# Kernel optimization log

Measured on AMD Instinct MI355X. Metric: run time of the kernel, lower is better.

## Reference

```python
import jax, jax.numpy as jnp
import numpy as np

N, P, Q, T, J, B, H = 262144, 64, 64, 2048, 512, 8, 64


def setup_inputs() -> dict:
    key = jax.random.key(0)
    ks = jax.random.split(key, 11)
    sH = 1.0 / np.sqrt(H).astype(np.float32)
    return {
        "idx": jax.random.randint(ks[0], (B,), 0, J),
        "seg_ids": jnp.sort(jax.random.randint(ks[1], (N,), 0, T)),
        "K": jax.random.normal(ks[2], (N, P), jnp.float32) * 0.1,
        "V": jax.random.normal(ks[3], (N, Q), jnp.float32),
        "S": jax.random.normal(ks[4], (P, J), jnp.float32) * 0.1,
        "W_ih": jax.random.normal(ks[5], (3 * H, Q), jnp.float32) * sH,
        "W_hh": jax.random.normal(ks[6], (3 * H, H), jnp.float32) * sH,
        "b_ih": jax.random.normal(ks[7], (3 * H,), jnp.float32) * sH,
        "b_hh": jax.random.normal(ks[8], (3 * H,), jnp.float32) * sH,
        "w_out": jax.random.normal(ks[9], (1, H), jnp.float32) * sH,
        "b_out": jax.random.normal(ks[10], (1,), jnp.float32) * sH,
    }


def reference(idx, seg_ids, K, V, S, W_ih, W_hh, b_ih, b_hh, w_out, b_out):
    # W[:, b] = K @ S[:, idx[b]]  -> [N, B]
    w = K @ S[:, idx]
    # ragged per-segment softmax over the N axis (segments = date windows)
    m = jax.ops.segment_max(w, seg_ids, num_segments=T)          # [T, B]
    e = jnp.exp(w - m[seg_ids])                                  # [N, B]
    denom = jax.ops.segment_sum(e, seg_ids, num_segments=T)     # [T, B]
    alpha = e / denom[seg_ids]                                   # [N, B]
    # weighted aggregation of V rows per segment: M[t, b] = sum_u alpha_u * V_u
    M = jax.ops.segment_sum(alpha[:, :, None] * V[:, None, :],
                            seg_ids, num_segments=T)             # [T, B, Q]
    X = jnp.transpose(M, (1, 0, 2))                              # [B, T, Q]

    # PyTorch GRU (gate order r,z,n). Faithful to the original bug: GRU was
    # built without batch_first=True, so axis 0 (B) is time, axis 1 (T) is batch.
    def step(h, x_t):  # x_t: [T, Q], h: [T, H]
        gi = x_t @ W_ih.T + b_ih                                 # [T, 3H]
        gh = h @ W_hh.T + b_hh                                   # [T, 3H]
        i_r, i_z, i_n = jnp.split(gi, 3, axis=1)
        h_r, h_z, h_n = jnp.split(gh, 3, axis=1)
        r = jax.nn.sigmoid(i_r + h_r)
        z = jax.nn.sigmoid(i_z + h_z)
        n = jnp.tanh(i_n + r * h_n)
        h_new = (1.0 - z) * n + z * h
        return h_new, h_new

    h0 = jnp.zeros((T, H), X.dtype)
    _, hs = jax.lax.scan(step, h0, X)                            # [B, T, H]
    preds = hs @ w_out.T + b_out                                 # [B, T, 1]
    return preds
```

## Files before the change

### kernel.cpp

```cpp
#include <hip/hip_runtime.h>
#include <math.h>

#define NN 262144
#define PP 64
#define QQ 64
#define TT 2048
#define JJ 512
#define BB 8
#define HH 64

__device__ __forceinline__ float lane_bcast(float v, int l) {
  return __int_as_float(__builtin_amdgcn_readlane(__float_as_int(v), l));
}

__global__ void k_prep(const int* __restrict__ seg_ids, int* __restrict__ seg_start) {
  int tid = blockIdx.x * blockDim.x + threadIdx.x;
  if (tid <= TT) {
    int lo = 0, hi = NN;
    while (lo < hi) {
      int mid = (lo + hi) >> 1;
      if (seg_ids[mid] < tid) lo = mid + 1; else hi = mid;
    }
    seg_start[tid] = lo;
  }
}

#define NPASS 6
__global__ __launch_bounds__(256) void k_fused2(const float* __restrict__ Kmat,
                                                const int* __restrict__ idx,
                                                const float* __restrict__ S,
                                                const float* __restrict__ V,
                                                const int* __restrict__ seg_start,
                                                float* __restrict__ M) {
  __shared__ __align__(16) float s_cols[BB * PP];
  __shared__ __align__(16) float accred[4][8][64];
  __shared__ float reds[4][8];
  int tid = threadIdx.x;
  int t = blockIdx.x;
  for (int i = tid; i < BB * PP; i += 256) {
    int p = i >> 3, b = i & 7;
    s_cols[b * PP + p] = S[p * JJ + idx[b]];
  }
  __syncthreads();

  int s = seg_start[t], e = seg_start[t + 1];
  int lane = tid & 63, j = tid >> 6;
  int len = e - s;
  int chunk = (len + 3) >> 2;
  int b0 = s + j * chunk;
  int b1 = b0 + chunk; if (b1 > e) b1 = e;

  int krow_in = lane >> 2;
  int sub = lane & 3;
  float ewa[NPASS], ewb[NPASS];
#pragma unroll
  for (int p = 0; p < NPASS; ++p) {
    ewa[p] = 0.f; ewb[p] = 0.f;
    int base = b0 + 16 * p;
    if (base < b1) {
      int rp = base + krow_in;
      int rc = (rp < b1) ? rp : (b1 - 1);
      const float4* Kp = reinterpret_cast<const float4*>(Kmat + (size_t)rc * PP + sub * 16);
      float4 kq[4];
#pragma unroll
      for (int jj = 0; jj < 4; ++jj) kq[jj] = Kp[jj];
      float a8[8];
#pragma unroll
      for (int b = 0; b < 8; ++b) a8[b] = 0.f;
#pragma unroll
      for (int j4 = 0; j4 < 4; ++j4) {
        float4 kk = kq[j4];
#pragma unroll
        for (int b = 0; b < 8; ++b) {
          const float4 sv = *reinterpret_cast<const float4*>(&s_cols[b * PP + sub * 16 + j4 * 4]);
          a8[b] += kk.x * sv.x + kk.y * sv.y + kk.z * sv.z + kk.w * sv.w;
        }
      }
#pragma unroll
      for (int b = 0; b < 8; ++b) {
        a8[b] += __shfl_xor(a8[b], 1);
        a8[b] += __shfl_xor(a8[b], 2);
      }
      float ox = (sub == 0) ? a8[0] : (sub == 1) ? a8[2] : (sub == 2) ? a8[4] : a8[6];
      float oy = (sub == 0) ? a8[1] : (sub == 1) ? a8[3] : (sub == 2) ? a8[5] : a8[7];
      ewa[p] = __expf(ox);
      ewb[p] = __expf(oy);
    }
  }

  int rsub = lane >> 4;
  int qg = lane & 15;
  float4 acc[8];
#pragma unroll
  for (int b = 0; b < 8; ++b) acc[b] = make_float4(0.f, 0.f, 0.f, 0.f);
  float4 selo = make_float4(0.f, 0.f, 0.f, 0.f);
  float4 sehi = make_float4(0.f, 0.f, 0.f, 0.f);

#pragma unroll
  for (int p = 0; p < NPASS; ++p) {
    int base = b0 + 16 * p;
    if (base < b1) {
#pragma unroll
      for (int q = 0; q < 4; ++q) {
        int qb = base + 4 * q;
        if (qb < b1) {
          int r = qb + rsub;
          float pr = (r < b1) ? 1.f : 0.f;
          int rc = (r < b1) ? r : (b1 - 1);
          float4 vv = reinterpret_cast<const float4*>(V + (size_t)rc * QQ)[qg];
          int sL = (4 * q + rsub) * 4;
          float e0 = __shfl(ewa[p], sL + 0), e1 = __shfl(ewb[p], sL + 0);
          float e2 = __shfl(ewa[p], sL + 1), e3 = __shfl(ewb[p], sL + 1);
          float e4 = __shfl(ewa[p], sL + 2), e5 = __shfl(ewb[p], sL + 2);
          float e6 = __shfl(ewa[p], sL + 3), e7 = __shfl(ewb[p], sL + 3);
          e0 *= pr; e1 *= pr; e2 *= pr; e3 *= pr;
          e4 *= pr; e5 *= pr; e6 *= pr; e7 *= pr;
          selo.x += e0; selo.y += e1; selo.z += e2; selo.w += e3;
          sehi.x += e4; sehi.y += e5; sehi.z += e6; sehi.w += e7;
          acc[0].x += e0 * vv.x; acc[0].y += e0 * vv.y; acc[0].z += e0 * vv.z; acc[0].w += e0 * vv.w;
          acc[1].x += e1 * vv.x; acc[1].y += e1 * vv.y; acc[1].z += e1 * vv.z; acc[1].w += e1 * vv.w;
          acc[2].x += e2 * vv.x; acc[2].y += e2 * vv.y; acc[2].z += e2 * vv.z; acc[2].w += e2 * vv.w;
          acc[3].x += e3 * vv.x; acc[3].y += e3 * vv.y; acc[3].z += e3 * vv.z; acc[3].w += e3 * vv.w;
          acc[4].x += e4 * vv.x; acc[4].y += e4 * vv.y; acc[4].z += e4 * vv.z; acc[4].w += e4 * vv.w;
          acc[5].x += e5 * vv.x; acc[5].y += e5 * vv.y; acc[5].z += e5 * vv.z; acc[5].w += e5 * vv.w;
          acc[6].x += e6 * vv.x; acc[6].y += e6 * vv.y; acc[6].z += e6 * vv.z; acc[6].w += e6 * vv.w;
          acc[7].x += e7 * vv.x; acc[7].y += e7 * vv.y; acc[7].z += e7 * vv.z; acc[7].w += e7 * vv.w;
        }
      }
    }
  }

#pragma unroll
  for (int b = 0; b < 8; ++b) {
    acc[b].x += __shfl_xor(acc[b].x, 16); acc[b].y += __shfl_xor(acc[b].y, 16);
    acc[b].z += __shfl_xor(acc[b].z, 16); acc[b].w += __shfl_xor(acc[b].w, 16);
    acc[b].x += __shfl_xor(acc[b].x, 32); acc[b].y += __shfl_xor(acc[b].y, 32);
    acc[b].z += __shfl_xor(acc[b].z, 32); acc[b].w += __shfl_xor(acc[b].w, 32);
  }
  selo.x += __shfl_xor(selo.x, 16); selo.y += __shfl_xor(selo.y, 16);
  selo.z += __shfl_xor(selo.z, 16); selo.w += __shfl_xor(selo.w, 16);
  sehi.x += __shfl_xor(sehi.x, 16); sehi.y += __shfl_xor(sehi.y, 16);
  sehi.z += __shfl_xor(sehi.z, 16); sehi.w += __shfl_xor(sehi.w, 16);
  selo.x += __shfl_xor(selo.x, 32); selo.y += __shfl_xor(selo.y, 32);
  selo.z += __shfl_xor(selo.z, 32); selo.w += __shfl_xor(selo.w, 32);
  sehi.x += __shfl_xor(sehi.x, 32); sehi.y += __shfl_xor(sehi.y, 32);
  sehi.z += __shfl_xor(sehi.z, 32); sehi.w += __shfl_xor(sehi.w, 32);

  if (rsub == 0) {
#pragma unroll
    for (int b = 0; b < 8; ++b)
      *reinterpret_cast<float4*>(&accred[j][b][qg * 4]) = acc[b];
    if (qg == 0) {
      reds[j][0] = selo.x; reds[j][1] = selo.y; reds[j][2] = selo.z; reds[j][3] = selo.w;
      reds[j][4] = sehi.x; reds[j][5] = sehi.y; reds[j][6] = sehi.z; reds[j][7] = sehi.w;
    }
  }
  __syncthreads();
  for (int o = tid; o < 512; o += 256) {
    int b = o >> 6, q = o & 63;
    float dd = reds[0][b] + reds[1][b] + reds[2][b] + reds[3][b];
    float inv = (dd > 0.f) ? 1.f / dd : 0.f;
    float sum = accred[0][b][q] + accred[1][b][q] + accred[2][b][q] + accred[3][b][q];
    M[(size_t)t * 512 + o] = sum * inv;
  }
}

__global__ __launch_bounds__(256) void k_gi(const float* __restrict__ M,
                                            const float* __restrict__ W_ih,
                                            const float* __restrict__ b_ih,
                                            float* __restrict__ GI) {
  __shared__ float Wt[64 * 193];
  int tid = threadIdx.x;
  for (int i = tid; i < 192 * 64; i += 256) {
    int g = i >> 6, k = i & 63;
    Wt[k * 193 + g] = W_ih[i];
  }
  __syncthreads();
  int lane = tid & 63, wv = tid >> 6;
  int row0 = blockIdx.x * 32 + wv * 8;
  float x[8];
#pragma unroll
  for (int rr = 0; rr < 8; ++rr) {
    int rho = row0 + rr;
    int b = rho >> 11, t = rho & 2047;
    x[rr] = M[((size_t)t * 8 + b) * 64 + lane];
  }
  float bi0 = b_ih[lane], bi1 = b_ih[64 + lane], bi2 = b_ih[128 + lane];
  float a0[8], a1[8], a2[8];
#pragma unroll
  for (int rr = 0; rr < 8; ++rr) { a0[rr] = bi0; a1[rr] = bi1; a2[rr] = bi2; }
#pragma unroll
  for (int k = 0; k < 64; ++k) {
    float w0 = Wt[k * 193 + lane];
    float w1 = Wt[k * 193 + 64 + lane];
    float w2 = Wt[k * 193 + 128 + lane];
#pragma unroll
    for (int rr = 0; rr < 8; ++rr) {
      float xk = lane_bcast(x[rr], k);
      a0[rr] += w0 * xk; a1[rr] += w1 * xk; a2[rr] += w2 * xk;
    }
  }
#pragma unroll
  for (int rr = 0; rr < 8; ++rr) {
    size_t rho = (size_t)row0 + rr;
    GI[rho * 192 + lane]       = a0[rr];
    GI[rho * 192 + 64 + lane]  = a1[rr];
    GI[rho * 192 + 128 + lane] = a2[rr];
  }
}

__global__ __launch_bounds__(256) void k_gru(const float* __restrict__ GI,
                                             const float* __restrict__ W_hh,
                                             const float* __restrict__ b_hh,
                                             const float* __restrict__ w_out,
                                             const float* __restrict__ b_out,
                                             float* __restrict__ preds) {
  __shared__ __align__(16) float Wl[192 * 68];
  int tid = threadIdx.x;
  for (int i = tid; i < 192 * 16; i += 256) {
    int g = i >> 4, c = i & 15;
    *reinterpret_cast<float4*>(&Wl[g * 68 + c * 4]) =
        *reinterpret_cast<const float4*>(W_hh + g * 64 + c * 4);
  }
  __syncthreads();
  int lane = tid & 63, wv = tid >> 6;
  int t = blockIdx.x * 4 + wv;
  float bh0 = b_hh[lane], bh1 = b_hh[64 + lane], bh2 = b_hh[128 + lane];
  float wo = w_out[lane];
  float bo = b_out[0];
  const float* w0base = &Wl[lane * 68];
  const float* w1base = &Wl[(64 + lane) * 68];
  const float* w2base = &Wl[(128 + lane) * 68];

  float gr[8], gz[8], gn[8];
#pragma unroll
  for (int b = 0; b < 8; ++b) {
    size_t base = ((size_t)b * TT + t) * 192;
    gr[b] = GI[base + lane];
    gz[b] = GI[base + 64 + lane];
    gn[b] = GI[base + 128 + lane];
  }

  float h;
  {
    float r = 1.f / (1.f + __expf(-(gr[0] + bh0)));
    float z = 1.f / (1.f + __expf(-(gz[0] + bh1)));
    float nv = tanhf(gn[0] + r * bh2);
    h = (1.f - z) * nv;
    float pv = h * wo;
#pragma unroll
    for (int off = 32; off; off >>= 1) pv += __shfl_xor(pv, off);
    if (lane == 0) preds[t] = pv + bo;
  }
#pragma unroll
  for (int b = 1; b < 8; ++b) {
    float ar = bh0, az = bh1, an = bh2;
#pragma unroll
    for (int c = 0; c < 16; ++c) {
      const float4 w0 = *reinterpret_cast<const float4*>(w0base + c * 4);
      const float4 w1 = *reinterpret_cast<const float4*>(w1base + c * 4);
      const float4 w2 = *reinterpret_cast<const float4*>(w2base + c * 4);
      float a0 = lane_bcast(h, c * 4 + 0), a1 = lane_bcast(h, c * 4 + 1);
      float a2 = lane_bcast(h, c * 4 + 2), a3 = lane_bcast(h, c * 4 + 3);
      ar += w0.x * a0 + w0.y * a1 + w0.z * a2 + w0.w * a3;
      az += w1.x * a0 + w1.y * a1 + w1.z * a2 + w1.w * a3;
      an += w2.x * a0 + w2.y * a1 + w2.z * a2 + w2.w * a3;
    }
    float r = 1.f / (1.f + __expf(-(gr[b] + ar)));
    float z = 1.f / (1.f + __expf(-(gz[b] + az)));
    float nv = tanhf(gn[b] + r * an);
    h = (1.f - z) * nv + z * h;
    float pv = h * wo;
#pragma unroll
    for (int off = 32; off; off >>= 1) pv += __shfl_xor(pv, off);
    if (lane == 0) preds[(size_t)b * TT + t] = pv + bo;
  }
}

extern "C" void kernel_launch(void* const* d_in, const int* in_sizes, int n_in,
                              void* d_out, int out_size, void* d_ws, size_t ws_size,
                              hipStream_t stream) {
  const int*   idx     = (const int*)d_in[0];
  const int*   seg_ids = (const int*)d_in[1];
  const float* Kmat    = (const float*)d_in[2];
  const float* V       = (const float*)d_in[3];
  const float* S       = (const float*)d_in[4];
  const float* W_ih    = (const float*)d_in[5];
  const float* W_hh    = (const float*)d_in[6];
  const float* b_ih    = (const float*)d_in[7];
  const float* b_hh    = (const float*)d_in[8];
  const float* w_out   = (const float*)d_in[9];
  const float* b_out   = (const float*)d_in[10];
  float* out = (float*)d_out;

  char* ws = (char*)d_ws;
  int*   seg_start = (int*)(ws + 0);
  float* M  = (float*)(ws + 8448);
  float* GI = (float*)(ws + 4202752);

  hipLaunchKernelGGL(k_prep, dim3(9), dim3(256), 0, stream, seg_ids, seg_start);
  hipLaunchKernelGGL(k_fused2, dim3(TT), dim3(256), 0, stream,
                     Kmat, idx, S, V, seg_start, M);
  hipLaunchKernelGGL(k_gi, dim3(512), dim3(256), 0, stream, M, W_ih, b_ih, GI);
  hipLaunchKernelGGL(k_gru, dim3(512), dim3(256), 0, stream, GI, W_hh, b_hh, w_out, b_out, out);
}
```

Measured before the change: 79.08 us.

## Split segment attention into fixed 64-row blocks with per-block partials and reduction

Replaces the per-segment block (one block per T, variable length) with fixed 64-row blocks over N, each producing up to 3 per-segment partial sums (weighted V and exp sums) into a workspace. A new reduction kernel then combines up to 4 block partials per segment and normalizes. The seg_start binary search is folded into the first kernel. This is meant to remove load imbalance and the NPASS cap, and to make K/V reads fully coalesced. In exchange it adds a ~25MB partial buffer write and read plus an extra launch, and it silently assumes each 64-row block spans at most 3 segments and each segment touches at most 4 blocks.

```diff
diff --git a/kernel.cpp b/kernel.cpp
--- a/kernel.cpp
+++ b/kernel.cpp
@@ -8,160 +8,189 @@
 #define JJ 512
 #define BB 8
 #define HH 64
+#define PSTR 520
 
 __device__ __forceinline__ float lane_bcast(float v, int l) {
   return __int_as_float(__builtin_amdgcn_readlane(__float_as_int(v), l));
 }
 
-__global__ void k_prep(const int* __restrict__ seg_ids, int* __restrict__ seg_start) {
-  int tid = blockIdx.x * blockDim.x + threadIdx.x;
-  if (tid <= TT) {
+__global__ __launch_bounds__(256) void k_fused3(const float* __restrict__ Kmat,
+                                                const int* __restrict__ idx,
+                                                const float* __restrict__ S,
+                                                const float* __restrict__ V,
+                                                const int* __restrict__ seg_ids,
+                                                float* __restrict__ P3,
+                                                int* __restrict__ seg_start) {
+  __shared__ __align__(16) float s_cols[BB * PP];
+  __shared__ __align__(16) float ew_lds[64 * 8];
+  __shared__ int seg_lds[64];
+  __shared__ __align__(16) float accred[4][8][64];
+  __shared__ float reds[4][8];
+  int tid = threadIdx.x;
+  int n0 = blockIdx.x * 64;
+  int gtid = blockIdx.x * 256 + tid;
+  if (gtid <= TT) {
     int lo = 0, hi = NN;
     while (lo < hi) {
       int mid = (lo + hi) >> 1;
-      if (seg_ids[mid] < tid) lo = mid + 1; else hi = mid;
-    }
-    seg_start[tid] = lo;
-  }
-}
-
-#define NPASS 6
-__global__ __launch_bounds__(256) void k_fused2(const float* __restrict__ Kmat,
-                                                const int* __restrict__ idx,
-                                                const float* __restrict__ S,
-                                                const float* __restrict__ V,
-                                                const int* __restrict__ seg_start,
-                                                float* __restrict__ M) {
-  __shared__ __align__(16) float s_cols[BB * PP];
-  __shared__ __align__(16) float accred[4][8][64];
-  __shared__ float reds[4][8];
-  int tid = threadIdx.x;
-  int t = blockIdx.x;
+      if (seg_ids[mid] < gtid) lo = mid + 1; else hi = mid;
+    }
+    seg_start[gtid] = lo;
+  }
+  if (tid < 64) seg_lds[tid] = seg_ids[n0 + tid];
   for (int i = tid; i < BB * PP; i += 256) {
     int p = i >> 3, b = i & 7;
     s_cols[b * PP + p] = S[p * JJ + idx[b]];
   }
-  __syncthreads();
-
+
+  int lane = tid & 63, w = tid >> 6;
+  int rsub = lane >> 4, qg = lane & 15;
+
+  float4 vv[4];
+#pragma unroll
+  for (int qi = 0; qi < 4; ++qi) {
+    int rl = w * 16 + qi * 4 + rsub;
+    vv[qi] = reinterpret_cast<const float4*>(V + (size_t)(n0 + rl) * QQ)[qg];
+  }
+  __syncthreads();
+
+  {
+    int row = tid >> 2;
+    int sub = tid & 3;
+    const float4* Kp = reinterpret_cast<const float4*>(Kmat + (size_t)(n0 + row) * PP + sub * 16);
+    float4 kq[4];
+#pragma unroll
+    for (int j = 0; j < 4; ++j) kq[j] = Kp[j];
+    float a8[8];
+#pragma unroll
+    for (int b = 0; b < 8; ++b) a8[b] = 0.f;
+#pragma unroll
+    for (int j4 = 0; j4 < 4; ++j4) {
+      float4 kk = kq[j4];
+#pragma unroll
+      for (int b = 0; b < 8; ++b) {
+        const float4 sv = *reinterpret_cast<const float4*>(&s_cols[b * PP + sub * 16 + j4 * 4]);
+        a8[b] += kk.x * sv.x + kk.y * sv.y + kk.z * sv.z + kk.w * sv.w;
+      }
+    }
+#pragma unroll
+    for (int b = 0; b < 8; ++b) {
+      a8[b] += __shfl_xor(a8[b], 1);
+      a8[b] += __shfl_xor(a8[b], 2);
+    }
+    float ox = (sub == 0) ? a8[0] : (sub == 1) ? a8[2] : (sub == 2) ? a8[4] : a8[6];
+    float oy = (sub == 0) ? a8[1] : (sub == 1) ? a8[3] : (sub == 2) ? a8[5] : a8[7];
+    *reinterpret_cast<float2*>(&ew_lds[row * 8 + 2 * sub]) =
+        make_float2(__expf(ox), __expf(oy));
+  }
+  __syncthreads();
+
+  int t_lo = seg_lds[0], t_hi = seg_lds[63];
+  int npass = t_hi - t_lo + 1; if (npass > 3) npass = 3;
+  int tq[4];
+#pragma unroll
+  for (int qi = 0; qi < 4; ++qi) tq[qi] = seg_lds[w * 16 + qi * 4 + rsub];
+
+  for (int pi = 0; pi < npass; ++pi) {
+    int tt = t_lo + pi;
+    float4 acc[8];
+#pragma unroll
+    for (int b = 0; b < 8; ++b) acc[b] = make_float4(0.f, 0.f, 0.f, 0.f);
+    float se[8];
+#pragma unroll
+    for (int b = 0; b < 8; ++b) se[b] = 0.f;
+#pragma unroll
+    for (int qi = 0; qi < 4; ++qi) {
+      int rl = w * 16 + qi * 4 + rsub;
+      float wq = (tq[qi] == tt) ? 1.f : 0.f;
+      float4 elo = *reinterpret_cast<const float4*>(&ew_lds[rl * 8]);
+      float4 ehi = *reinterpret_cast<const float4*>(&ew_lds[rl * 8 + 4]);
+      elo.x *= wq; elo.y *= wq; elo.z *= wq; elo.w *= wq;
+      ehi.x *= wq; ehi.y *= wq; ehi.z *= wq; ehi.w *= wq;
+      se[0] += elo.x; se[1] += elo.y; se[2] += elo.z; se[3] += elo.w;
+      se[4] += ehi.x; se[5] += ehi.y; se[6] += ehi.z; se[7] += ehi.w;
+      float4 v4 = vv[qi];
+      acc[0].x += elo.x * v4.x; acc[0].y += elo.x * v4.y; acc[0].z += elo.x * v4.z; acc[0].w += elo.x * v4.w;
+      acc[1].x += elo.y * v4.x; acc[1].y += elo.y * v4.y; acc[1].z += elo.y * v4.z; acc[1].w += elo.y * v4.w;
+      acc[2].x += elo.z * v4.x; acc[2].y += elo.z * v4.y; acc[2].z += elo.z * v4.z; acc[2].w += elo.z * v4.w;
+      acc[3].x += elo.w * v4.x; acc[3].y += elo.w * v4.y; acc[3].z += elo.w * v4.z; acc[3].w += elo.w * v4.w;
+      acc[4].x += ehi.x * v4.x; acc[4].y += ehi.x * v4.y; acc[4].z += ehi.x * v4.z; acc[4].w += ehi.x * v4.w;
+      acc[5].x += ehi.y * v4.x; acc[5].y += ehi.y * v4.y; acc[5].z += ehi.y * v4.z; acc[5].w += ehi.y * v4.w;
+      acc[6].x += ehi.z * v4.x; acc[6].y += ehi.z * v4.y; acc[6].z += ehi.z * v4.z; acc[6].w += ehi.z * v4.w;
+      acc[7].x += ehi.w * v4.x; acc[7].y += ehi.w * v4.y; acc[7].z += ehi.w * v4.z; acc[7].w += ehi.w * v4.w;
+    }
+#pragma unroll
+    for (int b = 0; b < 8; ++b) {
+      acc[b].x += __shfl_xor(acc[b].x, 16); acc[b].y += __shfl_xor(acc[b].y, 16);
+      acc[b].z += __shfl_xor(acc[b].z, 16); acc[b].w += __shfl_xor(acc[b].w, 16);
+      acc[b].x += __shfl_xor(acc[b].x, 32); acc[b].y += __shfl_xor(acc[b].y, 32);
+      acc[b].z += __shfl_xor(acc[b].z, 32); acc[b].w += __shfl_xor(acc[b].w, 32);
+      se[b] += __shfl_xor(se[b], 16);
+      se[b] += __shfl_xor(se[b], 32);
+    }
+    if (rsub == 0) {
+#pragma unroll
+      for (int b = 0; b < 8; ++b)
+        *reinterpret_cast<float4*>(&accred[w][b][qg * 4]) = acc[b];
+      if (qg == 0) {
+#pragma unroll
+        for (int b = 0; b < 8; ++b) reds[w][b] = se[b];
+      }
+    }
+    __syncthreads();
+    float* Pp = P3 + ((size_t)blockIdx.x * 3 + pi) * PSTR;
+    for (int o = tid; o < 512; o += 256) {
+      int b = o >> 6, q = o & 63;
+      Pp[o] = accred[0][b][q] + accred[1][b][q] + accred[2][b][q] + accred[3][b][q];
+    }
+    if (tid < 8)
+      Pp[512 + tid] = reds[0][tid] + reds[1][tid] + reds[2][tid] + reds[3][tid];
+    __syncthreads();
+  }
+}
+
+__global__ __launch_bounds__(256) void k_red(const float* __restrict__ P3,
+                                             const int* __restrict__ seg_start,
+                                             const int* __restrict__ seg_ids,
+                                             float* __restrict__ M) {
+  __shared__ float invL[8];
+  __shared__ int slotw[4];
+  int t = blockIdx.x, tid = threadIdx.x;
   int s = seg_start[t], e = seg_start[t + 1];
-  int lane = tid & 63, j = tid >> 6;
-  int len = e - s;
-  int chunk = (len + 3) >> 2;
-  int b0 = s + j * chunk;
-  int b1 = b0 + chunk; if (b1 > e) b1 = e;
-
-  int krow_in = lane >> 2;
-  int sub = lane & 3;
-  float ewa[NPASS], ewb[NPASS];
-#pragma unroll
-  for (int p = 0; p < NPASS; ++p) {
-    ewa[p] = 0.f; ewb[p] = 0.f;
-    int base = b0 + 16 * p;
-    if (base < b1) {
-      int rp = base + krow_in;
-      int rc = (rp < b1) ? rp : (b1 - 1);
-      const float4* Kp = reinterpret_cast<const float4*>(Kmat + (size_t)rc * PP + sub * 16);
-      float4 kq[4];
-#pragma unroll
-      for (int jj = 0; jj < 4; ++jj) kq[jj] = Kp[jj];
-      float a8[8];
-#pragma unroll
-      for (int b = 0; b < 8; ++b) a8[b] = 0.f;
-#pragma unroll
-      for (int j4 = 0; j4 < 4; ++j4) {
-        float4 kk = kq[j4];
-#pragma unroll
-        for (int b = 0; b < 8; ++b) {
-          const float4 sv = *reinterpret_cast<const float4*>(&s_cols[b * PP + sub * 16 + j4 * 4]);
-          a8[b] += kk.x * sv.x + kk.y * sv.y + kk.z * sv.z + kk.w * sv.w;
-        }
-      }
-#pragma unroll
-      for (int b = 0; b < 8; ++b) {
-        a8[b] += __shfl_xor(a8[b], 1);
-        a8[b] += __shfl_xor(a8[b], 2);
-      }
-      float ox = (sub == 0) ? a8[0] : (sub == 1) ? a8[2] : (sub == 2) ? a8[4] : a8[6];
-      float oy = (sub == 0) ? a8[1] : (sub == 1) ? a8[3] : (sub == 2) ? a8[5] : a8[7];
-      ewa[p] = __expf(ox);
-      ewb[p] = __expf(oy);
-    }
-  }
-
-  int rsub = lane >> 4;
-  int qg = lane & 15;
-  float4 acc[8];
-#pragma unroll
-  for (int b = 0; b < 8; ++b) acc[b] = make_float4(0.f, 0.f, 0.f, 0.f);
-  float4 selo = make_float4(0.f, 0.f, 0.f, 0.f);
-  float4 sehi = make_float4(0.f, 0.f, 0.f, 0.f);
-
-#pragma unroll
-  for (int p = 0; p < NPASS; ++p) {
-    int base = b0 + 16 * p;
-    if (base < b1) {
-#pragma unroll
-      for (int q = 0; q < 4; ++q) {
-        int qb = base + 4 * q;
-        if (qb < b1) {
-          int r = qb + rsub;
-          float pr = (r < b1) ? 1.f : 0.f;
-          int rc = (r < b1) ? r : (b1 - 1);
-          float4 vv = reinterpret_cast<const float4*>(V + (size_t)rc * QQ)[qg];
-          int sL = (4 * q + rsub) * 4;
-          float e0 = __shfl(ewa[p], sL + 0), e1 = __shfl(ewb[p], sL + 0);
-          float e2 = __shfl(ewa[p], sL + 1), e3 = __shfl(ewb[p], sL + 1);
-          float e4 = __shfl(ewa[p], sL + 2), e5 = __shfl(ewb[p], sL + 2);
-          float e6 = __shfl(ewa[p], sL + 3), e7 = __shfl(ewb[p], sL + 3);
-          e0 *= pr; e1 *= pr; e2 *= pr; e3 *= pr;
-          e4 *= pr; e5 *= pr; e6 *= pr; e7 *= pr;
-          selo.x += e0; selo.y += e1; selo.z += e2; selo.w += e3;
-          sehi.x += e4; sehi.y += e5; sehi.z += e6; sehi.w += e7;
-          acc[0].x += e0 * vv.x; acc[0].y += e0 * vv.y; acc[0].z += e0 * vv.z; acc[0].w += e0 * vv.w;
-          acc[1].x += e1 * vv.x; acc[1].y += e1 * vv.y; acc[1].z += e1 * vv.z; acc[1].w += e1 * vv.w;
-          acc[2].x += e2 * vv.x; acc[2].y += e2 * vv.y; acc[2].z += e2 * vv.z; acc[2].w += e2 * vv.w;
-          acc[3].x += e3 * vv.x; acc[3].y += e3 * vv.y; acc[3].z += e3 * vv.z; acc[3].w += e3 * vv.w;
-          acc[4].x += e4 * vv.x; acc[4].y += e4 * vv.y; acc[4].z += e4 * vv.z; acc[4].w += e4 * vv.w;
-          acc[5].x += e5 * vv.x; acc[5].y += e5 * vv.y; acc[5].z += e5 * vv.z; acc[5].w += e5 * vv.w;
-          acc[6].x += e6 * vv.x; acc[6].y += e6 * vv.y; acc[6].z += e6 * vv.z; acc[6].w += e6 * vv.w;
-          acc[7].x += e7 * vv.x; acc[7].y += e7 * vv.y; acc[7].z += e7 * vv.z; acc[7].w += e7 * vv.w;
-        }
-      }
-    }
-  }
-
-#pragma unroll
-  for (int b = 0; b < 8; ++b) {
-    acc[b].x += __shfl_xor(acc[b].x, 16); acc[b].y += __shfl_xor(acc[b].y, 16);
-    acc[b].z += __shfl_xor(acc[b].z, 16); acc[b].w += __shfl_xor(acc[b].w, 16);
-    acc[b].x += __shfl_xor(acc[b].x, 32); acc[b].y += __shfl_xor(acc[b].y, 32);
-    acc[b].z += __shfl_xor(acc[b].z, 32); acc[b].w += __shfl_xor(acc[b].w, 32);
-  }
-  selo.x += __shfl_xor(selo.x, 16); selo.y += __shfl_xor(selo.y, 16);
-  selo.z += __shfl_xor(selo.z, 16); selo.w += __shfl_xor(selo.w, 16);
-  sehi.x += __shfl_xor(sehi.x, 16); sehi.y += __shfl_xor(sehi.y, 16);
-  sehi.z += __shfl_xor(sehi.z, 16); sehi.w += __shfl_xor(sehi.w, 16);
-  selo.x += __shfl_xor(selo.x, 32); selo.y += __shfl_xor(selo.y, 32);
-  selo.z += __shfl_xor(selo.z, 32); selo.w += __shfl_xor(selo.w, 32);
-  sehi.x += __shfl_xor(sehi.x, 32); sehi.y += __shfl_xor(sehi.y, 32);
-  sehi.z += __shfl_xor(sehi.z, 32); sehi.w += __shfl_xor(sehi.w, 32);
-
-  if (rsub == 0) {
-#pragma unroll
-    for (int b = 0; b < 8; ++b)
-      *reinterpret_cast<float4*>(&accred[j][b][qg * 4]) = acc[b];
-    if (qg == 0) {
-      reds[j][0] = selo.x; reds[j][1] = selo.y; reds[j][2] = selo.z; reds[j][3] = selo.w;
-      reds[j][4] = sehi.x; reds[j][5] = sehi.y; reds[j][6] = sehi.z; reds[j][7] = sehi.w;
-    }
+  int w0 = s >> 6;
+  int nb = (e > s) ? (((e - 1) >> 6) - w0 + 1) : 0;
+  if (tid < 4) {
+    int valid = (tid < nb);
+    int wdx = valid ? (w0 + tid) : w0;
+    int tag = seg_ids[wdx * 64];
+    int slot = t - tag;
+    valid = valid && (slot >= 0) && (slot < 3);
+    slotw[tid] = valid ? (wdx * 3 + slot) : -1;
+  }
+  __syncthreads();
+  if (tid < 8) {
+    float dd = 0.f;
+#pragma unroll
+    for (int wi = 0; wi < 4; ++wi) {
+      int sw = slotw[wi];
+      int swc = (sw >= 0) ? sw : 0;
+      float v = P3[(size_t)swc * PSTR + 512 + tid];
+      dd += (sw >= 0) ? v : 0.f;
+    }
+    invL[tid] = (dd > 0.f) ? 1.f / dd : 0.f;
   }
   __syncthreads();
   for (int o = tid; o < 512; o += 256) {
-    int b = o >> 6, q = o & 63;
-    float dd = reds[0][b] + reds[1][b] + reds[2][b] + reds[3][b];
-    float inv = (dd > 0.f) ? 1.f / dd : 0.f;
-    float sum = accred[0][b][q] + accred[1][b][q] + accred[2][b][q] + accred[3][b][q];
-    M[(size_t)t * 512 + o] = sum * inv;
+    int b = o >> 6;
+    float sum = 0.f;
+#pragma unroll
+    for (int wi = 0; wi < 4; ++wi) {
+      int sw = slotw[wi];
+      int swc = (sw >= 0) ? sw : 0;
+      float v = P3[(size_t)swc * PSTR + o];
+      sum += (sw >= 0) ? v : 0.f;
+    }
+    M[(size_t)t * 512 + o] = sum * invL[b];
   }
 }
 
@@ -295,12 +324,13 @@
 
   char* ws = (char*)d_ws;
   int*   seg_start = (int*)(ws + 0);
-  float* M  = (float*)(ws + 8448);
-  float* GI = (float*)(ws + 4202752);
-
-  hipLaunchKernelGGL(k_prep, dim3(9), dim3(256), 0, stream, seg_ids, seg_start);
-  hipLaunchKernelGGL(k_fused2, dim3(TT), dim3(256), 0, stream,
-                     Kmat, idx, S, V, seg_start, M);
+  float* P3 = (float*)(ws + 8448);
+  float* M  = (float*)(ws + 25567488);
+  float* GI = (float*)(ws + 29761792);
+
+  hipLaunchKernelGGL(k_fused3, dim3(NN / 64), dim3(256), 0, stream,
+                     Kmat, idx, S, V, seg_ids, P3, seg_start);
+  hipLaunchKernelGGL(k_red, dim3(TT), dim3(256), 0, stream, P3, seg_start, seg_ids, M);
   hipLaunchKernelGGL(k_gi, dim3(512), dim3(256), 0, stream, M, W_ih, b_ih, GI);
   hipLaunchKernelGGL(k_gru, dim3(512), dim3(256), 0, stream, GI, W_hh, b_hh, w_out, b_out, out);
 }
```

New measurement: 88.26 us. 11.6% more time.
